# Performance work log

Measured on AMD Instinct MI355X. Metric: run time of the kernel, lower is better.

The kernel has to match this reference:

```python
import jax, jax.numpy as jnp
import numpy as np

HIDDEN = 256
NUM_NODES = 262144
NUM_GRAPHS = 4096
CHUNK_SIZE = 32  # hard-coded in the torch forward
NUM_CHUNKS = NUM_GRAPHS // CHUNK_SIZE


def setup_inputs() -> dict:
    key = jax.random.key(0)
    k1, k2, k3, k4 = jax.random.split(key, 4)
    x = jax.random.normal(k1, (NUM_NODES, HIDDEN), dtype=jnp.float32)
    # sorted graph ids covering all graphs 0..NUM_GRAPHS-1 (PyG batch vector)
    batch = (jnp.arange(NUM_NODES, dtype=jnp.int64) * NUM_GRAPHS) // NUM_NODES
    # attention MLP params: Linear(H,H) -> Tanh -> Linear(H,1, bias=False)
    s1 = 1.0 / np.sqrt(HIDDEN)
    W1 = jax.random.uniform(k2, (HIDDEN, HIDDEN), jnp.float32, -s1, s1)
    b1 = jax.random.uniform(k3, (HIDDEN,), jnp.float32, -s1, s1)
    W2 = jax.random.uniform(k4, (HIDDEN, 1), jnp.float32, -s1, s1)
    return {"x": x, "batch": batch, "W1": W1, "b1": b1, "W2": W2}


def reference(x, batch, W1, b1, W2):
    # attention scores: Linear -> Tanh -> Linear (no bias)  [N]
    scores = (jnp.tanh(x @ W1 + b1) @ W2)[:, 0]
    # softmax is over ALL nodes within each chunk of 32 consecutive graphs
    chunk_id = batch // CHUNK_SIZE
    m = jax.ops.segment_max(scores, chunk_id, num_segments=NUM_CHUNKS)
    e = jnp.exp(scores - m[chunk_id])
    denom = jax.ops.segment_sum(e, chunk_id, num_segments=NUM_CHUNKS)
    w = e / denom[chunk_id]  # [N]
    # global_add_pool of (w * x) per graph  -> [NUM_GRAPHS, HIDDEN]
    out = jax.ops.segment_sum(w[:, None] * x, batch, num_segments=NUM_GRAPHS)
    return out
```

## Files before the change

### kernel.cpp

```cpp
#include <hip/hip_runtime.h>

#define NODES 262144
#define HID 256
#define GRAPHS 4096
#define SROWS 64
#define TPB 8
#define NHALF (NODES / 32)
#define NSUP (NODES / SROWS)

typedef __attribute__((ext_vector_type(8))) short short8;
typedef __attribute__((ext_vector_type(4))) float floatx4;

__device__ __forceinline__ short bf16_rne(float f) {
  union { float f; unsigned int u; } v; v.f = f;
  unsigned int u = v.u;
  u += 0x7fffu + ((u >> 16) & 1u);
  return (short)(u >> 16);
}

__device__ __forceinline__ unsigned int cvt_pk_bf16(float lo, float hi) {
  unsigned int r;
  asm("v_cvt_pk_bf16_f32 %0, %1, %2" : "=v"(r) : "v"(lo), "v"(hi));
  return r;
}

__device__ __forceinline__ float bf16_to_f32(unsigned short u) {
  union { unsigned int u; float f; } v;
  v.u = ((unsigned int)u) << 16;
  return v.f;
}

__device__ __forceinline__ float fast_tanh(float x) {
  float e = exp2f(x * 2.885390082f);
  return 1.0f - 2.0f * __builtin_amdgcn_rcpf(e + 1.0f);
}

#define VBAR()                                                               \
  do {                                                                       \
    asm volatile("s_waitcnt vmcnt(8) lgkmcnt(0)" ::: "memory");              \
    __builtin_amdgcn_s_barrier();                                            \
  } while (0)
#define LBAR()                                                               \
  do {                                                                       \
    asm volatile("s_waitcnt lgkmcnt(0)" ::: "memory");                       \
    __builtin_amdgcn_s_barrier();                                            \
  } while (0)

__global__ __launch_bounds__(256) void k_prep(const float* __restrict__ w1,
                                              short* __restrict__ w1t) {
  __shared__ short t[64][65];
  const int bk = (blockIdx.x & 3) * 64;
  const int bn = (blockIdx.x >> 2) * 64;
  const int tx = threadIdx.x & 63, ty = threadIdx.x >> 6;
#pragma unroll
  for (int i = 0; i < 64; i += 4)
    t[tx][ty + i] = bf16_rne(w1[(bk + ty + i) * HID + bn + tx]);
  __syncthreads();
#pragma unroll
  for (int i = 0; i < 64; i += 4)
    w1t[(bn + ty + i) * HID + bk + tx] = t[ty + i][tx];
}


#define ISSUE(R, T)                                                          \
  do {                                                                       \
    const float4* xin_ =                                                     \
        ((const float4*)x) + (size_t)(sup0 + (T)) * (SROWS * 64);            \
    _Pragma("unroll") for (int i_ = 0; i_ < 4; ++i_) {                       \
      R[2 * i_]     = xin_[2 * tid + i_ * 1024];                             \
      R[2 * i_ + 1] = xin_[2 * tid + i_ * 1024 + 1];                         \
    }                                                                        \
  } while (0)

#define COMMIT(R)                                                            \
  do {                                                                       \
    _Pragma("unroll") for (int i_ = 0; i_ < 4; ++i_) {                       \
      int f_ = 2 * tid + i_ * 1024;                                          \
      int row_ = f_ >> 6, c4_ = f_ & 63;                                     \
      uint4 p_;                                                              \
      p_.x = cvt_pk_bf16(R[2 * i_].x, R[2 * i_].y);                          \
      p_.y = cvt_pk_bf16(R[2 * i_].z, R[2 * i_].w);                          \
      p_.z = cvt_pk_bf16(R[2 * i_ + 1].x, R[2 * i_ + 1].y);                  \
      p_.w = cvt_pk_bf16(R[2 * i_ + 1].z, R[2 * i_ + 1].w);                  \
      *(uint4*)&As[row_ * 264 + c4_ * 4] = p_;                               \
    }                                                                        \
  } while (0)

#define COMPUTE(T)                                                           \
  do {                                                                       \
    floatx4 acc[4][2];                                                       \
    _Pragma("unroll") for (int rt = 0; rt < 4; ++rt)                         \
        _Pragma("unroll") for (int ct = 0; ct < 2; ++ct)                     \
            _Pragma("unroll") for (int e = 0; e < 4; ++e) acc[rt][ct][e] = 0.f; \
    _Pragma("unroll") for (int kk = 0; kk < 8; ++kk) {                       \
      short8 afrag[4];                                                       \
      _Pragma("unroll") for (int rt = 0; rt < 4; ++rt)                       \
          afrag[rt] = *(const short8*)(abase + rt * 16 * 264 + kk * 32);     \
      _Pragma("unroll") for (int rt = 0; rt < 4; ++rt)                       \
          _Pragma("unroll") for (int ct = 0; ct < 2; ++ct)                   \
              acc[rt][ct] = __builtin_amdgcn_mfma_f32_16x16x32_bf16(         \
                  bfrag[kk][ct], afrag[rt], acc[rt][ct], 0, 0, 0);           \
    }                                                                        \
    _Pragma("unroll") for (int rt = 0; rt < 4; ++rt) {                       \
      float s_ = 0.f;                                                        \
      _Pragma("unroll") for (int ct = 0; ct < 2; ++ct)                       \
          _Pragma("unroll") for (int reg = 0; reg < 4; ++reg)                \
              s_ += fast_tanh(acc[rt][ct][reg] + b1q[ct][reg]) * w2q[ct][reg]; \
      s_ += __shfl_xor(s_, 16, 64);                                          \
      s_ += __shfl_xor(s_, 32, 64);                                          \
      if (quad == 0) part[wave][rt * 16 + l15] = s_;                         \
    }                                                                        \
    LBAR();             \
    if (wave < 2 && lane < 32) {                                             \
      int row_ = wave * 32 + lane;                                           \
      float s_ = 0.f;                                                        \
      _Pragma("unroll") for (int w_ = 0; w_ < 8; ++w_) s_ += part[w_][row_]; \
      float m_ = s_;                                                         \
      _Pragma("unroll") for (int mask = 1; mask < 32; mask <<= 1)            \
          m_ = fmaxf(m_, __shfl_xor(m_, mask, 32));                          \
      float e_ = __expf(s_ - m_);                                            \
      float l_ = e_;                                                         \
      _Pragma("unroll") for (int mask = 1; mask < 32; mask <<= 1)            \
          l_ += __shfl_xor(l_, mask, 32);                                    \
      wbuf[row_] = e_;                                                       \
      if (lane == 0) {                                                       \
        int h_ = 2 * (sup0 + (T)) + wave;                                    \
        mh[h_] = m_; lh[h_] = l_;                                            \
      }                                                                      \
    }                                                                        \
    LBAR();                                            \
    {                                                                        \
      const int halfsel_ = tid >> 8, col_ = tid & 255;                       \
      const int rbase_ = halfsel_ * 32;                                      \
      float pacc_ = 0.f;                                                     \
      _Pragma("unroll") for (int j_ = 0; j_ < 8; ++j_) {                     \
        float4 wv_ = *(const float4*)&wbuf[rbase_ + j_ * 4];                 \
        _Pragma("unroll") for (int q_ = 0; q_ < 4; ++q_) {                   \
          int i_ = rbase_ + j_ * 4 + q_;                                     \
          unsigned short u_ = *(const unsigned short*)&As[i_ * 264 + col_];  \
          float wq_ = (q_ == 0) ? wv_.x                                      \
                    : (q_ == 1) ? wv_.y                                      \
                    : (q_ == 2) ? wv_.z : wv_.w;                             \
          pacc_ = fmaf(wq_, bf16_to_f32(u_), pacc_);                         \
        }                                                                    \
      }                                                                      \
      Ah[(size_t)(2 * (sup0 + (T)) + halfsel_) * HID + col_] = pacc_;        \
    }                                                                        \
  } while (0)

__global__ __launch_bounds__(512, 2) void k_fused(
    const float* __restrict__ x, const short* __restrict__ w1t,
    const float* __restrict__ b1, const float* __restrict__ w2,
    float* __restrict__ Ah, float* __restrict__ mh, float* __restrict__ lh)
{
  __shared__ short As[SROWS * 264];
  __shared__ float part[8][SROWS];
  __shared__ float wbuf[SROWS];
  const int tid = threadIdx.x;
  const int wave = tid >> 6, lane = tid & 63;
  const int quad = lane >> 4, l15 = lane & 15;

  short8 bfrag[8][2];
  {
    const short* bbase = w1t + (wave * 32 + l15) * HID + quad * 8;
#pragma unroll
    for (int kk = 0; kk < 8; ++kk)
#pragma unroll
      for (int ct = 0; ct < 2; ++ct)
        bfrag[kk][ct] = *(const short8*)(bbase + ct * 16 * HID + kk * 32);
  }

  float b1q[2][4], w2q[2][4];
#pragma unroll
  for (int ct = 0; ct < 2; ++ct)
#pragma unroll
    for (int reg = 0; reg < 4; ++reg) {
      int n = wave * 32 + ct * 16 + quad * 4 + reg;
      b1q[ct][reg] = b1[n];
      w2q[ct][reg] = w2[n];
    }

  const short* abase = &As[l15 * 264 + quad * 8];

  const int sup0 = blockIdx.x * TPB;

  float4 rA[8], rB[8];
  ISSUE(rA, 0);
  ISSUE(rB, 1);

#pragma unroll 1
  for (int it = 0; it < TPB / 2; ++it) {
    const int t0 = 2 * it, t1 = 2 * it + 1;

    VBAR();
    COMMIT(rA);
    LBAR();
    if (t0 + 2 < TPB) ISSUE(rA, t0 + 2);
    COMPUTE(t0);

    VBAR();
    COMMIT(rB);
    LBAR();
    if (t1 + 2 < TPB) ISSUE(rB, t1 + 2);
    COMPUTE(t1);
  }
}

__global__ __launch_bounds__(256) void k_finish(
    const float* __restrict__ Ah, const float* __restrict__ mh,
    const float* __restrict__ lh, float* __restrict__ out)
{
  const int c = blockIdx.x >> 2, q = blockIdx.x & 3, t = threadIdx.x;
  __shared__ float sm[64], sl[64], sh[64];
  if (t < 64) { sm[t] = mh[c * 64 + t]; sl[t] = lh[c * 64 + t]; }
  __syncthreads();
  float m = sm[0];
#pragma unroll 8
  for (int j = 1; j < 64; ++j) m = fmaxf(m, sm[j]);
  float den = 0.f;
#pragma unroll 8
  for (int j = 0; j < 64; ++j) den += sl[j] * __expf(sm[j] - m);
  float inv = 1.0f / den;
  if (t < 64) sh[t] = __expf(sm[t] - m) * inv;
  __syncthreads();
  const float* ab = Ah + (size_t)c * 64 * HID;
#pragma unroll
  for (int jj = 0; jj < 8; ++jj) {
    int j = q * 8 + jj;
    float v = ab[(2 * j) * HID + t] * sh[2 * j] +
              ab[(2 * j + 1) * HID + t] * sh[2 * j + 1];
    out[((size_t)c * 32 + j) * HID + t] = v;
  }
}

extern "C" void kernel_launch(void* const* d_in, const int* in_sizes, int n_in,
                              void* d_out, int out_size, void* d_ws, size_t ws_size,
                              hipStream_t stream) {
  const float* x  = (const float*)d_in[0];
  const float* w1 = (const float*)d_in[2];
  const float* b1 = (const float*)d_in[3];
  const float* w2 = (const float*)d_in[4];
  float* out = (float*)d_out;

  char* ws = (char*)d_ws;
  float* Ah  = (float*)ws;
  float* mhb = (float*)(ws + (NHALF * HID) * 4);
  float* lhb = mhb + NHALF;
  short* w1t = (short*)(ws + (NHALF * HID + 2 * NHALF) * 4);

  k_prep  <<<16, 256, 0, stream>>>(w1, w1t);
  k_fused <<<NSUP / TPB, 512, 0, stream>>>(x, w1t, b1, w2, Ah, mhb, lhb);
  k_finish<<<GRAPHS / 8, 256, 0, stream>>>(Ah, mhb, lhb, out);
}
```

Baseline: 391.7 us.

## Single-buffer x prefetch and split GEMM into halves to raise occupancy

Replaces the two register buffers for x tiles with one, issuing the next tile's loads after the GEMM/epilogue instead of before it. The GEMM now runs as two passes of 32 rows, halving live accumulators, and launch bounds ask for 4 blocks per CU instead of 2. The aim is to cut VGPR pressure so more waves hide memory latency. In exchange there is less in-flight prefetch per wave, and the vmcnt wait is tightened, so the loads overlap less compute.

```diff
diff --git a/kernel.cpp b/kernel.cpp
--- a/kernel.cpp
+++ b/kernel.cpp
@@ -37,7 +37,7 @@
 
 #define VBAR()                                                               \
   do {                                                                       \
-    asm volatile("s_waitcnt vmcnt(8) lgkmcnt(0)" ::: "memory");              \
+    asm volatile("s_waitcnt vmcnt(1) lgkmcnt(0)" ::: "memory");              \
     __builtin_amdgcn_s_barrier();                                            \
   } while (0)
 #define LBAR()                                                               \
@@ -86,31 +86,39 @@
     }                                                                        \
   } while (0)
 
-#define COMPUTE(T)                                                           \
-  do {                                                                       \
-    floatx4 acc[4][2];                                                       \
-    _Pragma("unroll") for (int rt = 0; rt < 4; ++rt)                         \
+#define GEMM_EPI(T)                                                          \
+  do {                                                                       \
+    _Pragma("unroll") for (int ps = 0; ps < 2; ++ps) {                       \
+      floatx4 acc[2][2];                                                     \
+      _Pragma("unroll") for (int rr = 0; rr < 2; ++rr)                       \
+          _Pragma("unroll") for (int ct = 0; ct < 2; ++ct)                   \
+              _Pragma("unroll") for (int e = 0; e < 4; ++e)                  \
+                  acc[rr][ct][e] = 0.f;                                      \
+      _Pragma("unroll") for (int kk = 0; kk < 8; ++kk) {                     \
+        short8 afrag[2];                                                     \
+        _Pragma("unroll") for (int rr = 0; rr < 2; ++rr)                     \
+            afrag[rr] =                                                      \
+                *(const short8*)(abase + (ps * 2 + rr) * 16 * 264 + kk * 32);\
+        _Pragma("unroll") for (int rr = 0; rr < 2; ++rr)                     \
+            _Pragma("unroll") for (int ct = 0; ct < 2; ++ct)                 \
+                acc[rr][ct] = __builtin_amdgcn_mfma_f32_16x16x32_bf16(       \
+                    bfrag[kk][ct], afrag[rr], acc[rr][ct], 0, 0, 0);         \
+      }                                                                      \
+      _Pragma("unroll") for (int rr = 0; rr < 2; ++rr) {                     \
+        float s_ = 0.f;                                                      \
         _Pragma("unroll") for (int ct = 0; ct < 2; ++ct)                     \
-            _Pragma("unroll") for (int e = 0; e < 4; ++e) acc[rt][ct][e] = 0.f; \
-    _Pragma("unroll") for (int kk = 0; kk < 8; ++kk) {                       \
-      short8 afrag[4];                                                       \
-      _Pragma("unroll") for (int rt = 0; rt < 4; ++rt)                       \
-          afrag[rt] = *(const short8*)(abase + rt * 16 * 264 + kk * 32);     \
-      _Pragma("unroll") for (int rt = 0; rt < 4; ++rt)                       \
-          _Pragma("unroll") for (int ct = 0; ct < 2; ++ct)                   \
-              acc[rt][ct] = __builtin_amdgcn_mfma_f32_16x16x32_bf16(         \
-                  bfrag[kk][ct], afrag[rt], acc[rt][ct], 0, 0, 0);           \
-    }                                                                        \
-    _Pragma("unroll") for (int rt = 0; rt < 4; ++rt) {                       \
-      float s_ = 0.f;                                                        \
-      _Pragma("unroll") for (int ct = 0; ct < 2; ++ct)                       \
-          _Pragma("unroll") for (int reg = 0; reg < 4; ++reg)                \
-              s_ += fast_tanh(acc[rt][ct][reg] + b1q[ct][reg]) * w2q[ct][reg]; \
-      s_ += __shfl_xor(s_, 16, 64);                                          \
-      s_ += __shfl_xor(s_, 32, 64);                                          \
-      if (quad == 0) part[wave][rt * 16 + l15] = s_;                         \
-    }                                                                        \
-    LBAR();             \
+            _Pragma("unroll") for (int reg = 0; reg < 4; ++reg)              \
+                s_ += fast_tanh(acc[rr][ct][reg] + b1q[ct][reg]) *           \
+                      w2q[ct][reg];                                          \
+        s_ += __shfl_xor(s_, 16, 64);                                        \
+        s_ += __shfl_xor(s_, 32, 64);                                        \
+        if (quad == 0) part[wave][(ps * 2 + rr) * 16 + l15] = s_;            \
+      }                                                                      \
+    }                                                                        \
+  } while (0)
+
+#define STATS_POOL(T)                                                        \
+  do {                                                                       \
     if (wave < 2 && lane < 32) {                                             \
       int row_ = wave * 32 + lane;                                           \
       float s_ = 0.f;                                                        \
@@ -148,7 +156,7 @@
     }                                                                        \
   } while (0)
 
-__global__ __launch_bounds__(512, 2) void k_fused(
+__global__ __launch_bounds__(512, 4) void k_fused(
     const float* __restrict__ x, const short* __restrict__ w1t,
     const float* __restrict__ b1, const float* __restrict__ w2,
     float* __restrict__ Ah, float* __restrict__ mh, float* __restrict__ lh)
@@ -184,25 +192,19 @@
 
   const int sup0 = blockIdx.x * TPB;
 
-  float4 rA[8], rB[8];
-  ISSUE(rA, 0);
-  ISSUE(rB, 1);
+  float4 r[8];
+  ISSUE(r, 0);
+  asm volatile("s_waitcnt vmcnt(0)" ::: "memory");
 
 #pragma unroll 1
-  for (int it = 0; it < TPB / 2; ++it) {
-    const int t0 = 2 * it, t1 = 2 * it + 1;
-
+  for (int tt = 0; tt < TPB; ++tt) {
     VBAR();
-    COMMIT(rA);
+    COMMIT(r);
     LBAR();
-    if (t0 + 2 < TPB) ISSUE(rA, t0 + 2);
-    COMPUTE(t0);
-
-    VBAR();
-    COMMIT(rB);
+    GEMM_EPI(tt);
+    if (tt + 1 < TPB) ISSUE(r, tt + 1);
     LBAR();
-    if (t1 + 2 < TPB) ISSUE(rB, t1 + 2);
-    COMPUTE(t1);
+    STATS_POOL(tt);
   }
 }
 
```

Measured after the change: 452.8 us. 15.6% more time.
